# Kernel optimization log

Measured on AMD Instinct MI355X. Metric: run time of the kernel, lower is better.

Reference implementation:

```python
import jax, jax.numpy as jnp
from jax import lax
import numpy as np

GAMMA = 0.25        # inv_temp
C_SCALE = 1.0       # spectral_scale
STRIDE = 8          # patch stride (== patch_size, non-overlapping)


def setup_inputs() -> dict:
    key = jax.random.key(0)
    ks = jax.random.split(key, 9)
    B, C, H = 1024, 3, 64
    D, NP, M, NH, R, P = 256, 64, 1024, 8, 32, 8
    return {
        "x": jax.random.normal(ks[0], (B, C, H, H), jnp.float32),
        "z": jax.random.normal(ks[1], (B, NP, D), jnp.float32),
        "encoder_weight": jax.random.normal(ks[2], (D, C, P, P), jnp.float32) * 0.05,
        "encoder_bias": jax.random.normal(ks[3], (D,), jnp.float32) * 0.05,
        "visible_bias": jax.random.normal(ks[4], (C, H, H), jnp.float32) * 0.05,
        "pos_bias": jax.random.normal(ks[5], (NP, D), jnp.float32) * 0.05,
        "memory_weight": jax.random.normal(ks[6], (D, M), jnp.float32) * 0.05,
        "W_Q": jax.random.normal(ks[7], (NH, R, D), jnp.float32) * 0.05,
        "W_K": jax.random.normal(ks[8], (NH, R, D), jnp.float32) * 0.05,
    }


def reference(x, z, encoder_weight, encoder_bias, visible_bias, pos_bias,
              memory_weight, W_Q, W_K):
    """E = 0.5||x||^2 + 0.5||z||^2 - Phi_coupling(x, z); returns (B,)."""
    B = x.shape[0]
    D = encoder_weight.shape[0]

    quad_x = 0.5 * jnp.sum(x * x, axis=(1, 2, 3))
    quad_z = 0.5 * jnp.sum(z * z, axis=(1, 2))

    # visible-bias coupling
    phi_vis = jnp.sum(visible_bias[None] * x, axis=(1, 2, 3))

    # conv encode: (B, D, gh, gw) -> (B, NP, D)
    enc = lax.conv_general_dilated(
        x, C_SCALE * encoder_weight, window_strides=(STRIDE, STRIDE),
        padding='VALID', dimension_numbers=('NCHW', 'OIHW', 'NCHW'))
    encoded = enc.reshape(B, D, -1).transpose(0, 2, 1)  # (B, NP, D)

    # enc_act = 'none' -> identity
    phi_enc = jnp.sum(encoded * z, axis=(1, 2))
    phi_bias = jnp.sum(z * encoder_bias, axis=(1, 2))
    phi_pos = jnp.sum(z * pos_bias[None], axis=(1, 2))

    # memory ReLU^2 term: (B, NP, M)
    mem_proj = jnp.einsum('bpd,dm->bpm', z, C_SCALE * memory_weight)
    phi_mem = jnp.sum(jnp.square(jax.nn.relu(mem_proj)), axis=(1, 2))

    # Hopfield attention logsumexp term
    Q = jnp.einsum('bpd,hrd->bhrp', z, C_SCALE * W_Q)  # (B, H, R, NP)
    K = jnp.einsum('bpd,hrd->bhrp', z, C_SCALE * W_K)
    A = jnp.einsum('bhdm,bhdn->bhmn', Q, K)            # (B, H, NP, NP)
    phi_att = jnp.sum(jax.scipy.special.logsumexp(GAMMA * A, axis=-1),
                      axis=(1, 2)) / GAMMA

    coupling = phi_vis + phi_enc + phi_bias + phi_pos + phi_mem + phi_att
    return quad_x + quad_z - coupling
```

## Files before the change

### kernel.cpp

```cpp
#include <hip/hip_runtime.h>
#include <hip/hip_bf16.h>

#define GAMMA 0.25f


typedef __attribute__((ext_vector_type(8))) short short8;
typedef __attribute__((ext_vector_type(4))) float f32x4;

__device__ __forceinline__ float dot4(float4 a, float4 b) {
  return fmaf(a.x, b.x, fmaf(a.y, b.y, fmaf(a.z, b.z, a.w * b.w)));
}

__device__ __forceinline__ void fma4(float4& a, float s, float4 w) {
  a.x = fmaf(s, w.x, a.x); a.y = fmaf(s, w.y, a.y);
  a.z = fmaf(s, w.z, a.z); a.w = fmaf(s, w.w, a.w);
}

__device__ __forceinline__ ushort f2bf(float f) {
  __hip_bfloat16 h = __float2bfloat16(f);
  return *reinterpret_cast<ushort*>(&h);
}

__device__ __forceinline__ float bf2f(ushort u) {
  union { unsigned int i; float f; } v;
  v.i = ((unsigned int)u) << 16;
  return v.f;
}

__device__ __forceinline__ float block_sum_256(float v, float* tmp) {
#pragma unroll
  for (int off = 32; off; off >>= 1) v += __shfl_down(v, off, 64);
  int w = threadIdx.x >> 6;
  if ((threadIdx.x & 63) == 0) tmp[w] = v;
  __syncthreads();
  return tmp[0] + tmp[1] + tmp[2] + tmp[3];
}

__global__ __launch_bounds__(256) void k_cvt_weights_v5(
    const float* __restrict__ wq, const float* __restrict__ wk,
    const float* __restrict__ ew, const float* __restrict__ mw,
    ushort* __restrict__ wcf, ushort* __restrict__ ewt,
    ushort* __restrict__ mtf) {
  int bid = blockIdx.x, t = threadIdx.x;
  if (bid < 64) {
    int tid = bid * 256 + t;
    int frag = tid >> 6, l = tid & 63;
    int ctg = frag >> 3, kc = frag & 7;
    int col = ctg * 16 + (l & 15);
    int h = col >> 6, qk = (col >> 5) & 1, rr = col & 31;
    int k0 = kc * 32 + (l >> 4) * 8;
    const float* s = (qk ? wk : wq) + ((size_t)h * 32 + rr) * 256 + k0;
    float4 u = *(const float4*)s;
    float4 v = *(const float4*)(s + 4);
    ushort o[8];
    o[0] = f2bf(u.x); o[1] = f2bf(u.y); o[2] = f2bf(u.z); o[3] = f2bf(u.w);
    o[4] = f2bf(v.x); o[5] = f2bf(v.y); o[6] = f2bf(v.z); o[7] = f2bf(v.w);
    *(ushort4*)(wcf + (size_t)tid * 8) = *(ushort4*)&o[0];
    *(ushort4*)(wcf + (size_t)tid * 8 + 4) = *(ushort4*)&o[4];
  } else if (bid < 88) {
    int tid = (bid - 64) * 256 + t;
    int frag = tid >> 6, l = tid & 63;
    int ks = frag / 12, ct = frag % 12;
    const float* s = ew + (size_t)(ks * 32 + (l >> 4) * 8) * 192 +
                     ct * 16 + (l & 15);
    ushort o[8];
#pragma unroll
    for (int i = 0; i < 8; ++i) o[i] = f2bf(s[(size_t)i * 192]);
    *(ushort4*)(ewt + (size_t)tid * 8) = *(ushort4*)&o[0];
    *(ushort4*)(ewt + (size_t)tid * 8 + 4) = *(ushort4*)&o[4];
  } else {
    __shared__ ushort tile[32][264];
    int bid2 = bid - 88;
    int kc = bid2 >> 2, mg = bid2 & 3;
#pragma unroll
    for (int j = 0; j < 8; ++j) {
      int idx = t + j * 256;
      int kl = idx >> 6, m4 = idx & 63;
      float4 v = *(const float4*)(mw + (size_t)(kc * 32 + kl) * 1024 +
                                  mg * 256 + m4 * 4);
      ushort* dst = &tile[kl][m4 * 4];
      dst[0] = f2bf(v.x); dst[1] = f2bf(v.y);
      dst[2] = f2bf(v.z); dst[3] = f2bf(v.w);
    }
    __syncthreads();
#pragma unroll
    for (int j = 0; j < 4; ++j) {
      int e = t + j * 256;
      int fl = e >> 6, l2 = e & 63;
      int frag = (mg * 16 + fl) * 8 + kc;
      int m_loc = fl * 16 + (l2 & 15);
      ushort o[8];
#pragma unroll
      for (int i = 0; i < 8; ++i) o[i] = tile[(l2 >> 4) * 8 + i][m_loc];
      *(ushort4*)(mtf + ((size_t)frag * 64 + l2) * 8) = *(ushort4*)&o[0];
      *(ushort4*)(mtf + ((size_t)frag * 64 + l2) * 8 + 4) = *(ushort4*)&o[4];
    }
  }
}

__global__ __launch_bounds__(256) void k_mega(
    const float* __restrict__ z, const float* __restrict__ eb,
    const float* __restrict__ pb, const ushort* __restrict__ mtf,
    const ushort* __restrict__ wcf, float* __restrict__ out) {
  __shared__ ushort SL[32768];
  const int t = threadIdx.x, l = t & 63, w = t >> 6;
  const int b = blockIdx.x;
  const int q = l >> 4, m = l & 15;
  float s = 0.f;

  {
    const float4* zb4 = (const float4*)(z + (size_t)b * 16384);
    const float4* pb4 = (const float4*)pb;
    const float4* eb4 = (const float4*)eb;
#pragma unroll
    for (int n = 0; n < 16; ++n) {
      int i = t + n * 256;
      float4 zv = zb4[i];
      float4 pv = pb4[i];
      float4 ev = eb4[i & 63];
      float4 c;
      c.x = pv.x + ev.x; c.y = pv.y + ev.y;
      c.z = pv.z + ev.z; c.w = pv.w + ev.w;
      s += 0.5f * dot4(zv, zv) - dot4(zv, c);
      int p = i >> 6, d4 = i & 63;
      int ks = d4 >> 3, sub = (d4 & 7) >> 1, e0 = (d4 & 1) * 4;
      int li = (p & 15) + sub * 16;
      ushort4 o;
      o.x = f2bf(zv.x); o.y = f2bf(zv.y); o.z = f2bf(zv.z); o.w = f2bf(zv.w);
      *(ushort4*)(SL + (size_t)(((p >> 4) * 8 + ks) * 64 + li) * 8 + e0) = o;
    }
  }
  __syncthreads();

#pragma unroll 1
  for (int ct = 0; ct < 4; ++ct) {
    const ushort* Bb = mtf + ((size_t)(ct * 16 + w * 4) * 8) * 512 +
                       (size_t)l * 8;
    short8 fb[2][4];
#pragma unroll
    for (int c = 0; c < 4; ++c) fb[0][c] = *(const short8*)(Bb + (c * 8 + 0) * 512);
#pragma unroll
    for (int c = 0; c < 4; ++c) fb[1][c] = *(const short8*)(Bb + (c * 8 + 1) * 512);

    f32x4 acc[4][4];
#pragma unroll
    for (int r = 0; r < 4; ++r)
#pragma unroll
      for (int c = 0; c < 4; ++c) acc[r][c] = f32x4{0.f, 0.f, 0.f, 0.f};

#pragma unroll
    for (int kc = 0; kc < 8; ++kc) {
      const int cur = kc & 1;
      short8 a4[4];
#pragma unroll
      for (int r = 0; r < 4; ++r)
        a4[r] = *(const short8*)(SL + (size_t)((r * 8 + kc) * 64 + l) * 8);
#pragma unroll
      for (int r = 0; r < 4; ++r)
#pragma unroll
        for (int c = 0; c < 4; ++c)
          acc[r][c] = __builtin_amdgcn_mfma_f32_16x16x32_bf16(a4[r], fb[cur][c],
                                                              acc[r][c], 0, 0, 0);
      if (kc < 6) {
#pragma unroll
        for (int c = 0; c < 4; ++c)
          fb[cur][c] = *(const short8*)(Bb + (c * 8 + kc + 2) * 512);
      }
    }
#pragma unroll
    for (int r = 0; r < 4; ++r)
#pragma unroll
      for (int c = 0; c < 4; ++c)
#pragma unroll
        for (int e = 0; e < 4; ++e) {
          float rr = fmaxf(acc[r][c][e], 0.f);
          s -= rr * rr;
        }
  }

  float part = 0.f;
  char* dstg = (char*)(SL + 16384);
#pragma unroll 1
  for (int half = 0; half < 2; ++half) {
    const ushort* Bb = wcf + ((size_t)((half * 16 + w * 4) * 8)) * 512 +
                       (size_t)l * 8;
    short8 fb[2][4];
#pragma unroll
    for (int c = 0; c < 4; ++c) fb[0][c] = *(const short8*)(Bb + (c * 8 + 0) * 512);
#pragma unroll
    for (int c = 0; c < 4; ++c) fb[1][c] = *(const short8*)(Bb + (c * 8 + 1) * 512);

    f32x4 acc[4][4];
#pragma unroll
    for (int r = 0; r < 4; ++r)
#pragma unroll
      for (int c = 0; c < 4; ++c) acc[r][c] = f32x4{0.f, 0.f, 0.f, 0.f};

#pragma unroll
    for (int kc = 0; kc < 8; ++kc) {
      const int cur = kc & 1;
      short8 a4[4];
#pragma unroll
      for (int r = 0; r < 4; ++r)
        a4[r] = *(const short8*)(SL + (size_t)((r * 8 + kc) * 64 + l) * 8);
#pragma unroll
      for (int r = 0; r < 4; ++r)
#pragma unroll
        for (int c = 0; c < 4; ++c)
          acc[r][c] = __builtin_amdgcn_mfma_f32_16x16x32_bf16(a4[r], fb[cur][c],
                                                              acc[r][c], 0, 0, 0);
      if (kc < 6) {
#pragma unroll
        for (int c = 0; c < 4; ++c)
          fb[cur][c] = *(const short8*)(Bb + (c * 8 + kc + 2) * 512);
      }
    }

#pragma unroll
    for (int rt = 0; rt < 4; ++rt)
#pragma unroll
      for (int c = 0; c < 4; ++c)
#pragma unroll
        for (int reg = 0; reg < 4; ++reg) {
          int row = 16 * rt + 4 * q + reg;
          int col = (4 * w + c) * 16 + m;
          int ba = ((row * 256 + col) * 2) ^ ((row & 7) << 4);
          *(ushort*)(dstg + ba) = f2bf(acc[rt][c][reg]);
        }
    __syncthreads();

#pragma unroll
    for (int hh = 0; hh < 4; ++hh) {
      int rowq = 16 * w + m;
      short8 qa = *(const short8*)(
          dstg + (((rowq * 256 + hh * 64 + q * 8) * 2) ^ ((rowq & 7) << 4)));
      f32x4 a2[4];
#pragma unroll
      for (int nt = 0; nt < 4; ++nt) {
        int rowk = 16 * nt + m;
        short8 kb = *(const short8*)(
            dstg + (((rowk * 256 + hh * 64 + 32 + q * 8) * 2) ^ ((rowk & 7) << 4)));
        a2[nt] = __builtin_amdgcn_mfma_f32_16x16x32_bf16(
            qa, kb, f32x4{0.f, 0.f, 0.f, 0.f}, 0, 0, 0);
      }
#pragma unroll
      for (int reg = 0; reg < 4; ++reg) {
        float e = __expf(GAMMA * a2[0][reg]) + __expf(GAMMA * a2[1][reg]) +
                  __expf(GAMMA * a2[2][reg]) + __expf(GAMMA * a2[3][reg]);
        e += __shfl_xor(e, 1, 64);
        e += __shfl_xor(e, 2, 64);
        e += __shfl_xor(e, 4, 64);
        e += __shfl_xor(e, 8, 64);
        part += (m == 0) ? __logf(e) : 0.f;
      }
    }
    __syncthreads();
  }
  s -= part * (1.0f / GAMMA);

  float r = block_sum_256(s, (float*)SL);
  if (t == 0) out[b] = r;
}

__global__ __launch_bounds__(256) void k_enc_v5(
    const float* __restrict__ x, const float* __restrict__ vb,
    const float* __restrict__ z, const ushort* __restrict__ ewt,
    float* __restrict__ out) {
  __shared__ ushort xs[12288];
  __shared__ ushort ebuf[2][6144];
  __shared__ float tmp[4];
  const int b = blockIdx.x, t = threadIdx.x, l = t & 63, w = t >> 6;
  const int q = l >> 4, m = l & 15;

  const float* Zr = z + (size_t)b * 16384 + (size_t)(16 * w + m) * 256 + q * 8;
  short8 a[8];
#pragma unroll
  for (int ks = 0; ks < 8; ++ks) {
    float4 u = *(const float4*)(Zr + ks * 32);
    float4 v = *(const float4*)(Zr + ks * 32 + 4);
    ushort o[8];
    o[0] = f2bf(u.x); o[1] = f2bf(u.y); o[2] = f2bf(u.z); o[3] = f2bf(u.w);
    o[4] = f2bf(v.x); o[5] = f2bf(v.y); o[6] = f2bf(v.z); o[7] = f2bf(v.w);
    a[ks] = *(short8*)o;
  }

  short8 st[3];
#pragma unroll
  for (int i = 0; i < 3; ++i)
    st[i] = *(const short8*)(ewt + (size_t)(t + i * 256) * 8);

  const float4* xb = (const float4*)(x + (size_t)b * 12288);
  const float4* vb4 = (const float4*)vb;
  ushort4* xs4 = (ushort4*)xs;
  float s = 0.f;
  for (int i = t; i < 3072; i += 256) {
    float4 xv = xb[i];
    float4 bv = vb4[i];
    s += 0.5f * dot4(xv, xv) - dot4(bv, xv);
    ushort4 o;
    o.x = f2bf(xv.x); o.y = f2bf(xv.y); o.z = f2bf(xv.z); o.w = f2bf(xv.w);
    xs4[i] = o;
  }
#pragma unroll
  for (int i = 0; i < 3; ++i)
    *(short8*)(ebuf[0] + (size_t)(t + i * 256) * 8) = st[i];
  __syncthreads();

  f32x4 acc[12];
#pragma unroll
  for (int ct = 0; ct < 12; ++ct) acc[ct] = f32x4{0.f, 0.f, 0.f, 0.f};

#pragma unroll
  for (int ks = 0; ks < 8; ++ks) {
    const int cur = ks & 1;
    if (ks < 7) {
#pragma unroll
      for (int i = 0; i < 3; ++i)
        st[i] = *(const short8*)(ewt + (size_t)(ks + 1) * 6144 +
                                 (size_t)(t + i * 256) * 8);
    }
#pragma unroll
    for (int ct = 0; ct < 12; ++ct) {
      short8 bv = *(const short8*)(ebuf[cur] + (size_t)(ct * 64 + l) * 8);
      acc[ct] = __builtin_amdgcn_mfma_f32_16x16x32_bf16(a[ks], bv, acc[ct], 0, 0, 0);
    }
    if (ks < 7) {
#pragma unroll
      for (int i = 0; i < 3; ++i)
        *(short8*)(ebuf[cur ^ 1] + (size_t)(t + i * 256) * 8) = st[i];
    }
    __syncthreads();
  }

#pragma unroll
  for (int ct = 0; ct < 12; ++ct) {
#pragma unroll
    for (int reg = 0; reg < 4; ++reg) {
      const int p = 16 * w + 4 * q + reg, gi = p >> 3, gj = p & 7;
      const int k = ct * 16 + m, c = k >> 6, r2 = k & 63;
      const int ii = r2 >> 3, jj = r2 & 7;
      s -= acc[ct][reg] * bf2f(xs[c * 4096 + (gi * 8 + ii) * 64 + gj * 8 + jj]);
    }
  }
  float r = block_sum_256(s, tmp);
  if (t == 0) atomicAdd(out + b, r);
}

__global__ __launch_bounds__(256) void k_xz(const float* __restrict__ x,
                                            const float* __restrict__ z,
                                            const float* __restrict__ vb,
                                            const float* __restrict__ eb,
                                            const float* __restrict__ pb,
                                            float* __restrict__ out) {
  __shared__ float tmp[4];
  int b = blockIdx.x, t = threadIdx.x;
  const float4* xb = (const float4*)(x + (size_t)b * 12288);
  const float4* vb4 = (const float4*)vb;
  float s = 0.f;
  for (int i = t; i < 3072; i += 256) {
    float4 xv = xb[i];
    float4 bv = vb4[i];
    s += 0.5f * dot4(xv, xv) - dot4(bv, xv);
  }
  const float4* zb = (const float4*)(z + (size_t)b * 16384);
  const float4* pb4 = (const float4*)pb;
  const float4* eb4 = (const float4*)eb;
  for (int i = t; i < 4096; i += 256) {
    float4 zv = zb[i];
    float4 pv = pb4[i];
    float4 ev = eb4[i & 63];
    float4 c;
    c.x = pv.x + ev.x; c.y = pv.y + ev.y; c.z = pv.z + ev.z; c.w = pv.w + ev.w;
    s += 0.5f * dot4(zv, zv) - dot4(zv, c);
  }
  float r = block_sum_256(s, tmp);
  if (t == 0) out[b] = r;
}

__global__ __launch_bounds__(256) void k_enc(const float* __restrict__ x,
                                             const float* __restrict__ z,
                                             const float* __restrict__ ew,
                                             float* __restrict__ out) {
  __shared__ float xs[12288];
  __shared__ float tmp[4];
  int b = blockIdx.x, t = threadIdx.x;
  const float4* xb4 = (const float4*)(x + (size_t)b * 12288);
  for (int i = t; i < 3072; i += 256) ((float4*)xs)[i] = xb4[i];
  __syncthreads();

  float acc[64];
#pragma unroll
  for (int p = 0; p < 64; ++p) acc[p] = 0.f;

  for (int k4 = 0; k4 < 48; ++k4) {
    float4 wv = *(const float4*)(ew + (size_t)t * 192 + k4 * 4);
    int c = k4 >> 4;
    int ii = (k4 >> 1) & 7;
    int jh = (k4 & 1) * 4;
    const float* base = xs + c * 4096 + ii * 64 + jh;
#pragma unroll
    for (int p = 0; p < 64; ++p) {
      float4 pv = *(const float4*)(base + (p >> 3) * 512 + (p & 7) * 8);
      acc[p] = fmaf(wv.x, pv.x,
               fmaf(wv.y, pv.y, fmaf(wv.z, pv.z, fmaf(wv.w, pv.w, acc[p]))));
    }
  }
  const float* zb = z + (size_t)b * 16384;
  float s = 0.f;
#pragma unroll
  for (int p = 0; p < 64; ++p) s += acc[p] * zb[p * 256 + t];
  float r = block_sum_256(s, tmp);
  if (t == 0) atomicAdd(out + b, -r);
}

__global__ __launch_bounds__(256) void k_mem(const float* __restrict__ z,
                                             const float* __restrict__ mw,
                                             float* __restrict__ out) {
  __shared__ float zs[16 * 256];
  __shared__ float tmp[4];
  int b = blockIdx.x >> 2, pt = blockIdx.x & 3, t = threadIdx.x;
  const float4* zb4 = (const float4*)(z + (size_t)b * 16384 + pt * 4096);
  for (int i = t; i < 1024; i += 256) ((float4*)zs)[i] = zb4[i];
  __syncthreads();

  const float4* m4 = (const float4*)mw;
  float4 acc[16];
#pragma unroll
  for (int pp = 0; pp < 16; ++pp) acc[pp] = make_float4(0.f, 0.f, 0.f, 0.f);

#pragma unroll 2
  for (int k4 = 0; k4 < 64; ++k4) {
    float4 w0 = m4[(4 * k4 + 0) * 256 + t];
    float4 w1 = m4[(4 * k4 + 1) * 256 + t];
    float4 w2 = m4[(4 * k4 + 2) * 256 + t];
    float4 w3 = m4[(4 * k4 + 3) * 256 + t];
#pragma unroll
    for (int pp = 0; pp < 16; ++pp) {
      float4 zv = *(const float4*)&zs[pp * 256 + k4 * 4];
      fma4(acc[pp], zv.x, w0);
      fma4(acc[pp], zv.y, w1);
      fma4(acc[pp], zv.z, w2);
      fma4(acc[pp], zv.w, w3);
    }
  }
  float total = 0.f;
#pragma unroll
  for (int pp = 0; pp < 16; ++pp) {
    float r;
    r = fmaxf(acc[pp].x, 0.f); total = fmaf(r, r, total);
    r = fmaxf(acc[pp].y, 0.f); total = fmaf(r, r, total);
    r = fmaxf(acc[pp].z, 0.f); total = fmaf(r, r, total);
    r = fmaxf(acc[pp].w, 0.f); total = fmaf(r, r, total);
  }
  float r = block_sum_256(total, tmp);
  if (t == 0) atomicAdd(out + b, -r);
}

__global__ __launch_bounds__(256) void k_attn(const float* __restrict__ z,
                                              const float* __restrict__ wq,
                                              const float* __restrict__ wk,
                                              float* __restrict__ out) {
  __shared__ float lds[8192];
  __shared__ float red[4];
  const int b = blockIdx.x >> 1, half = blockIdx.x & 1;
  const int t = threadIdx.x;
  const int lane = t & 63;
  const int w = __builtin_amdgcn_readfirstlane(t >> 6);
  const float4* zb4 = (const float4*)(z + (size_t)b * 16384);

  float qa[4][8], ka[4][8];
#pragma unroll
  for (int hh = 0; hh < 4; ++hh)
#pragma unroll
    for (int j = 0; j < 8; ++j) { qa[hh][j] = 0.f; ka[hh][j] = 0.f; }

  float4* lds4 = (float4*)lds;
  for (int dc = 0; dc < 2; ++dc) {
    __syncthreads();
    for (int i = t; i < 2048; i += 256) {
      int p = i >> 5, ld4 = i & 31;
      lds4[ld4 * 64 + (p ^ (ld4 & 7))] = zb4[p * 64 + dc * 32 + ld4];
    }
    __syncthreads();
#pragma unroll
    for (int hh = 0; hh < 4; ++hh) {
      int h = half * 4 + hh;
      const float* Wqb = wq + (size_t)h * 8192 + (size_t)(w * 8) * 256 + dc * 128;
      const float* Wkb = wk + (size_t)h * 8192 + (size_t)(w * 8) * 256 + dc * 128;
      for (int ld4 = 0; ld4 < 32; ++ld4) {
        float4 wv[8], kv[8];
#pragma unroll
        for (int j = 0; j < 8; ++j) {
          wv[j] = *(const float4*)(Wqb + j * 256 + ld4 * 4);
          kv[j] = *(const float4*)(Wkb + j * 256 + ld4 * 4);
        }
        float4 zv = lds4[ld4 * 64 + (lane ^ (ld4 & 7))];
#pragma unroll
        for (int j = 0; j < 8; ++j) {
          qa[hh][j] = fmaf(wv[j].x, zv.x, fmaf(wv[j].y, zv.y,
                      fmaf(wv[j].z, zv.z, fmaf(wv[j].w, zv.w, qa[hh][j]))));
          ka[hh][j] = fmaf(kv[j].x, zv.x, fmaf(kv[j].y, zv.y,
                      fmaf(kv[j].z, zv.z, fmaf(kv[j].w, zv.w, ka[hh][j]))));
        }
      }
    }
  }

  float* Qs = lds;
  float* Ks = lds + 2048;
  float lse = 0.f;
#pragma unroll
  for (int hh = 0; hh < 4; ++hh) {
    __syncthreads();
#pragma unroll
    for (int j = 0; j < 8; ++j) {
      Qs[(w * 8 + j) * 64 + lane] = qa[hh][j];
      Ks[(w * 8 + j) * 64 + lane] = ka[hh][j];
    }
    __syncthreads();
    float av[16];
#pragma unroll
    for (int mm = 0; mm < 16; ++mm) av[mm] = 0.f;
    for (int rr = 0; rr < 32; ++rr) {
      float kv = Ks[rr * 64 + lane];
      const float* qrow = &Qs[rr * 64 + w * 16];
      float4 q0 = *(const float4*)(qrow + 0);
      float4 q1 = *(const float4*)(qrow + 4);
      float4 q2 = *(const float4*)(qrow + 8);
      float4 q3 = *(const float4*)(qrow + 12);
      av[0]  = fmaf(q0.x, kv, av[0]);  av[1]  = fmaf(q0.y, kv, av[1]);
      av[2]  = fmaf(q0.z, kv, av[2]);  av[3]  = fmaf(q0.w, kv, av[3]);
      av[4]  = fmaf(q1.x, kv, av[4]);  av[5]  = fmaf(q1.y, kv, av[5]);
      av[6]  = fmaf(q1.z, kv, av[6]);  av[7]  = fmaf(q1.w, kv, av[7]);
      av[8]  = fmaf(q2.x, kv, av[8]);  av[9]  = fmaf(q2.y, kv, av[9]);
      av[10] = fmaf(q2.z, kv, av[10]); av[11] = fmaf(q2.w, kv, av[11]);
      av[12] = fmaf(q3.x, kv, av[12]); av[13] = fmaf(q3.y, kv, av[13]);
      av[14] = fmaf(q3.z, kv, av[14]); av[15] = fmaf(q3.w, kv, av[15]);
    }
#pragma unroll
    for (int mm = 0; mm < 16; ++mm) {
      float e = __expf(GAMMA * av[mm]);
#pragma unroll
      for (int off = 32; off; off >>= 1) e += __shfl_xor(e, off, 64);
      lse += __logf(e);
    }
  }
  if (lane == 0) red[w] = lse;
  __syncthreads();
  if (t == 0)
    atomicAdd(out + b, -(red[0] + red[1] + red[2] + red[3]) * (1.0f / GAMMA));
}

extern "C" void kernel_launch(void* const* d_in, const int* in_sizes, int n_in,
                              void* d_out, int out_size, void* d_ws,
                              size_t ws_size, hipStream_t stream) {
  (void)in_sizes; (void)n_in; (void)out_size;
  const float* x  = (const float*)d_in[0];
  const float* z  = (const float*)d_in[1];
  const float* ew = (const float*)d_in[2];
  const float* eb = (const float*)d_in[3];
  const float* vb = (const float*)d_in[4];
  const float* pb = (const float*)d_in[5];
  const float* mw = (const float*)d_in[6];
  const float* wq = (const float*)d_in[7];
  const float* wk = (const float*)d_in[8];
  float* out = (float*)d_out;

  const size_t MT_B = (size_t)1024 * 256 * 2;
  const size_t WC_B = (size_t)512 * 256 * 2;
  const size_t EW_B = (size_t)96 * 64 * 8 * 2;
  const size_t FULL = MT_B + WC_B + EW_B;

  ushort* mtf = (ushort*)d_ws;
  ushort* wcf = (ushort*)((char*)d_ws + MT_B);
  ushort* ewt = (ushort*)((char*)d_ws + MT_B + WC_B);

  if (ws_size >= FULL) {
    k_cvt_weights_v5<<<120, 256, 0, stream>>>(wq, wk, ew, mw, wcf, ewt, mtf);
    k_mega  <<<1024, 256, 0, stream>>>(z, eb, pb, mtf, wcf, out);
    k_enc_v5<<<1024, 256, 0, stream>>>(x, vb, z, ewt, out);
  } else {
    k_xz  <<<1024, 256, 0, stream>>>(x, z, vb, eb, pb, out);
    k_enc <<<1024, 256, 0, stream>>>(x, z, ew, out);
    k_mem <<<4096, 256, 0, stream>>>(z, mw, out);
    k_attn<<<2048, 256, 0, stream>>>(z, wq, wk, out);
  }
}
```

Measured before the change: 221.6 us.

## Merge memory/attention and encoder kernels into one launch with interleaved block roles

Combines the mega (memory + attention) kernel and the encoder kernel into a single 2048-block launch. The block index picks the role and the batch, interleaving groups of 8 blocks so both kinds of work run at the same time on the GPU. Both roles now accumulate into the output with atomicAdd, which requires a memset of the output first. The aim is to drop a launch and its tail, and to overlap the MFMA-heavy blocks with the load-heavy ones. The cost is an extra memset and atomic traffic on every output, and both roles must share one LDS and register allocation.

```diff
diff --git a/kernel.cpp b/kernel.cpp
--- a/kernel.cpp
+++ b/kernel.cpp
@@ -98,250 +98,248 @@
   }
 }
 
-__global__ __launch_bounds__(256) void k_mega(
-    const float* __restrict__ z, const float* __restrict__ eb,
-    const float* __restrict__ pb, const ushort* __restrict__ mtf,
-    const ushort* __restrict__ wcf, float* __restrict__ out) {
+__global__ __launch_bounds__(256) void k_fused(
+    const float* __restrict__ x, const float* __restrict__ z,
+    const float* __restrict__ eb, const float* __restrict__ vb,
+    const float* __restrict__ pb, const ushort* __restrict__ ewt,
+    const ushort* __restrict__ mtf, const ushort* __restrict__ wcf,
+    float* __restrict__ out) {
   __shared__ ushort SL[32768];
+  __shared__ float tmp[4];
   const int t = threadIdx.x, l = t & 63, w = t >> 6;
-  const int b = blockIdx.x;
+  const int bid = blockIdx.x;
+  const int type = (bid >> 3) & 1;
+  const int b = ((bid >> 4) << 3) | (bid & 7);
   const int q = l >> 4, m = l & 15;
   float s = 0.f;
 
-  {
-    const float4* zb4 = (const float4*)(z + (size_t)b * 16384);
-    const float4* pb4 = (const float4*)pb;
-    const float4* eb4 = (const float4*)eb;
-#pragma unroll
-    for (int n = 0; n < 16; ++n) {
-      int i = t + n * 256;
-      float4 zv = zb4[i];
-      float4 pv = pb4[i];
-      float4 ev = eb4[i & 63];
-      float4 c;
-      c.x = pv.x + ev.x; c.y = pv.y + ev.y;
-      c.z = pv.z + ev.z; c.w = pv.w + ev.w;
-      s += 0.5f * dot4(zv, zv) - dot4(zv, c);
-      int p = i >> 6, d4 = i & 63;
-      int ks = d4 >> 3, sub = (d4 & 7) >> 1, e0 = (d4 & 1) * 4;
-      int li = (p & 15) + sub * 16;
+  if (type == 0) {
+    {
+      const float4* zb4 = (const float4*)(z + (size_t)b * 16384);
+      const float4* pb4 = (const float4*)pb;
+      const float4* eb4 = (const float4*)eb;
+#pragma unroll
+      for (int n = 0; n < 16; ++n) {
+        int i = t + n * 256;
+        float4 zv = zb4[i];
+        float4 pv = pb4[i];
+        float4 ev = eb4[i & 63];
+        float4 c;
+        c.x = pv.x + ev.x; c.y = pv.y + ev.y;
+        c.z = pv.z + ev.z; c.w = pv.w + ev.w;
+        s += 0.5f * dot4(zv, zv) - dot4(zv, c);
+        int p = i >> 6, d4 = i & 63;
+        int ks = d4 >> 3, sub = (d4 & 7) >> 1, e0 = (d4 & 1) * 4;
+        int li = (p & 15) + sub * 16;
+        ushort4 o;
+        o.x = f2bf(zv.x); o.y = f2bf(zv.y); o.z = f2bf(zv.z); o.w = f2bf(zv.w);
+        *(ushort4*)(SL + (size_t)(((p >> 4) * 8 + ks) * 64 + li) * 8 + e0) = o;
+      }
+    }
+    __syncthreads();
+
+#pragma unroll 1
+    for (int ct = 0; ct < 4; ++ct) {
+      const ushort* Bb = mtf + ((size_t)(ct * 16 + w * 4) * 8) * 512 +
+                         (size_t)l * 8;
+      short8 fb[2][4];
+#pragma unroll
+      for (int c = 0; c < 4; ++c) fb[0][c] = *(const short8*)(Bb + (c * 8 + 0) * 512);
+#pragma unroll
+      for (int c = 0; c < 4; ++c) fb[1][c] = *(const short8*)(Bb + (c * 8 + 1) * 512);
+
+      f32x4 acc[4][4];
+#pragma unroll
+      for (int r = 0; r < 4; ++r)
+#pragma unroll
+        for (int c = 0; c < 4; ++c) acc[r][c] = f32x4{0.f, 0.f, 0.f, 0.f};
+
+#pragma unroll
+      for (int kc = 0; kc < 8; ++kc) {
+        const int cur = kc & 1;
+        short8 a4[4];
+#pragma unroll
+        for (int r = 0; r < 4; ++r)
+          a4[r] = *(const short8*)(SL + (size_t)((r * 8 + kc) * 64 + l) * 8);
+#pragma unroll
+        for (int r = 0; r < 4; ++r)
+#pragma unroll
+          for (int c = 0; c < 4; ++c)
+            acc[r][c] = __builtin_amdgcn_mfma_f32_16x16x32_bf16(a4[r], fb[cur][c],
+                                                                acc[r][c], 0, 0, 0);
+        if (kc < 6) {
+#pragma unroll
+          for (int c = 0; c < 4; ++c)
+            fb[cur][c] = *(const short8*)(Bb + (c * 8 + kc + 2) * 512);
+        }
+      }
+#pragma unroll
+      for (int r = 0; r < 4; ++r)
+#pragma unroll
+        for (int c = 0; c < 4; ++c)
+#pragma unroll
+          for (int e = 0; e < 4; ++e) {
+            float rr = fmaxf(acc[r][c][e], 0.f);
+            s -= rr * rr;
+          }
+    }
+
+    float part = 0.f;
+    char* dstg = (char*)(SL + 16384);
+#pragma unroll 1
+    for (int half = 0; half < 2; ++half) {
+      const ushort* Bb = wcf + ((size_t)((half * 16 + w * 4) * 8)) * 512 +
+                         (size_t)l * 8;
+      short8 fb[2][4];
+#pragma unroll
+      for (int c = 0; c < 4; ++c) fb[0][c] = *(const short8*)(Bb + (c * 8 + 0) * 512);
+#pragma unroll
+      for (int c = 0; c < 4; ++c) fb[1][c] = *(const short8*)(Bb + (c * 8 + 1) * 512);
+
+      f32x4 acc[4][4];
+#pragma unroll
+      for (int r = 0; r < 4; ++r)
+#pragma unroll
+        for (int c = 0; c < 4; ++c) acc[r][c] = f32x4{0.f, 0.f, 0.f, 0.f};
+
+#pragma unroll
+      for (int kc = 0; kc < 8; ++kc) {
+        const int cur = kc & 1;
+        short8 a4[4];
+#pragma unroll
+        for (int r = 0; r < 4; ++r)
+          a4[r] = *(const short8*)(SL + (size_t)((r * 8 + kc) * 64 + l) * 8);
+#pragma unroll
+        for (int r = 0; r < 4; ++r)
+#pragma unroll
+          for (int c = 0; c < 4; ++c)
+            acc[r][c] = __builtin_amdgcn_mfma_f32_16x16x32_bf16(a4[r], fb[cur][c],
+                                                                acc[r][c], 0, 0, 0);
+        if (kc < 6) {
+#pragma unroll
+          for (int c = 0; c < 4; ++c)
+            fb[cur][c] = *(const short8*)(Bb + (c * 8 + kc + 2) * 512);
+        }
+      }
+
+#pragma unroll
+      for (int rt = 0; rt < 4; ++rt)
+#pragma unroll
+        for (int c = 0; c < 4; ++c)
+#pragma unroll
+          for (int reg = 0; reg < 4; ++reg) {
+            int row = 16 * rt + 4 * q + reg;
+            int col = (4 * w + c) * 16 + m;
+            int ba = ((row * 256 + col) * 2) ^ ((row & 7) << 4);
+            *(ushort*)(dstg + ba) = f2bf(acc[rt][c][reg]);
+          }
+      __syncthreads();
+
+#pragma unroll
+      for (int hh = 0; hh < 4; ++hh) {
+        int rowq = 16 * w + m;
+        short8 qa = *(const short8*)(
+            dstg + (((rowq * 256 + hh * 64 + q * 8) * 2) ^ ((rowq & 7) << 4)));
+        f32x4 a2[4];
+#pragma unroll
+        for (int nt = 0; nt < 4; ++nt) {
+          int rowk = 16 * nt + m;
+          short8 kb = *(const short8*)(
+              dstg + (((rowk * 256 + hh * 64 + 32 + q * 8) * 2) ^ ((rowk & 7) << 4)));
+          a2[nt] = __builtin_amdgcn_mfma_f32_16x16x32_bf16(
+              qa, kb, f32x4{0.f, 0.f, 0.f, 0.f}, 0, 0, 0);
+        }
+#pragma unroll
+        for (int reg = 0; reg < 4; ++reg) {
+          float e = __expf(GAMMA * a2[0][reg]) + __expf(GAMMA * a2[1][reg]) +
+                    __expf(GAMMA * a2[2][reg]) + __expf(GAMMA * a2[3][reg]);
+          e += __shfl_xor(e, 1, 64);
+          e += __shfl_xor(e, 2, 64);
+          e += __shfl_xor(e, 4, 64);
+          e += __shfl_xor(e, 8, 64);
+          part += (m == 0) ? __logf(e) : 0.f;
+        }
+      }
+      __syncthreads();
+    }
+    s -= part * (1.0f / GAMMA);
+  } else {
+    ushort* xs    = SL;
+    ushort* ebuf0 = SL + 12288;
+    ushort* ebuf1 = SL + 18432;
+
+    const float* Zr = z + (size_t)b * 16384 + (size_t)(16 * w + m) * 256 + q * 8;
+    short8 a[8];
+#pragma unroll
+    for (int ks = 0; ks < 8; ++ks) {
+      float4 u = *(const float4*)(Zr + ks * 32);
+      float4 v = *(const float4*)(Zr + ks * 32 + 4);
+      ushort o[8];
+      o[0] = f2bf(u.x); o[1] = f2bf(u.y); o[2] = f2bf(u.z); o[3] = f2bf(u.w);
+      o[4] = f2bf(v.x); o[5] = f2bf(v.y); o[6] = f2bf(v.z); o[7] = f2bf(v.w);
+      a[ks] = *(short8*)o;
+    }
+
+    short8 st[3];
+#pragma unroll
+    for (int i = 0; i < 3; ++i)
+      st[i] = *(const short8*)(ewt + (size_t)(t + i * 256) * 8);
+
+    const float4* xb = (const float4*)(x + (size_t)b * 12288);
+    const float4* vb4 = (const float4*)vb;
+    ushort4* xs4 = (ushort4*)xs;
+    for (int i = t; i < 3072; i += 256) {
+      float4 xv = xb[i];
+      float4 bv = vb4[i];
+      s += 0.5f * dot4(xv, xv) - dot4(bv, xv);
       ushort4 o;
-      o.x = f2bf(zv.x); o.y = f2bf(zv.y); o.z = f2bf(zv.z); o.w = f2bf(zv.w);
-      *(ushort4*)(SL + (size_t)(((p >> 4) * 8 + ks) * 64 + li) * 8 + e0) = o;
-    }
-  }
-  __syncthreads();
-
-#pragma unroll 1
-  for (int ct = 0; ct < 4; ++ct) {
-    const ushort* Bb = mtf + ((size_t)(ct * 16 + w * 4) * 8) * 512 +
-                       (size_t)l * 8;
-    short8 fb[2][4];
-#pragma unroll
-    for (int c = 0; c < 4; ++c) fb[0][c] = *(const short8*)(Bb + (c * 8 + 0) * 512);
-#pragma unroll
-    for (int c = 0; c < 4; ++c) fb[1][c] = *(const short8*)(Bb + (c * 8 + 1) * 512);
-
-    f32x4 acc[4][4];
-#pragma unroll
-    for (int r = 0; r < 4; ++r)
-#pragma unroll
-      for (int c = 0; c < 4; ++c) acc[r][c] = f32x4{0.f, 0.f, 0.f, 0.f};
-
-#pragma unroll
-    for (int kc = 0; kc < 8; ++kc) {
-      const int cur = kc & 1;
-      short8 a4[4];
-#pragma unroll
-      for (int r = 0; r < 4; ++r)
-        a4[r] = *(const short8*)(SL + (size_t)((r * 8 + kc) * 64 + l) * 8);
-#pragma unroll
-      for (int r = 0; r < 4; ++r)
-#pragma unroll
-        for (int c = 0; c < 4; ++c)
-          acc[r][c] = __builtin_amdgcn_mfma_f32_16x16x32_bf16(a4[r], fb[cur][c],
-                                                              acc[r][c], 0, 0, 0);
-      if (kc < 6) {
-#pragma unroll
-        for (int c = 0; c < 4; ++c)
-          fb[cur][c] = *(const short8*)(Bb + (c * 8 + kc + 2) * 512);
-      }
-    }
-#pragma unroll
-    for (int r = 0; r < 4; ++r)
-#pragma unroll
-      for (int c = 0; c < 4; ++c)
-#pragma unroll
-        for (int e = 0; e < 4; ++e) {
-          float rr = fmaxf(acc[r][c][e], 0.f);
-          s -= rr * rr;
-        }
-  }
-
-  float part = 0.f;
-  char* dstg = (char*)(SL + 16384);
-#pragma unroll 1
-  for (int half = 0; half < 2; ++half) {
-    const ushort* Bb = wcf + ((size_t)((half * 16 + w * 4) * 8)) * 512 +
-                       (size_t)l * 8;
-    short8 fb[2][4];
-#pragma unroll
-    for (int c = 0; c < 4; ++c) fb[0][c] = *(const short8*)(Bb + (c * 8 + 0) * 512);
-#pragma unroll
-    for (int c = 0; c < 4; ++c) fb[1][c] = *(const short8*)(Bb + (c * 8 + 1) * 512);
-
-    f32x4 acc[4][4];
-#pragma unroll
-    for (int r = 0; r < 4; ++r)
-#pragma unroll
-      for (int c = 0; c < 4; ++c) acc[r][c] = f32x4{0.f, 0.f, 0.f, 0.f};
-
-#pragma unroll
-    for (int kc = 0; kc < 8; ++kc) {
-      const int cur = kc & 1;
-      short8 a4[4];
-#pragma unroll
-      for (int r = 0; r < 4; ++r)
-        a4[r] = *(const short8*)(SL + (size_t)((r * 8 + kc) * 64 + l) * 8);
-#pragma unroll
-      for (int r = 0; r < 4; ++r)
-#pragma unroll
-        for (int c = 0; c < 4; ++c)
-          acc[r][c] = __builtin_amdgcn_mfma_f32_16x16x32_bf16(a4[r], fb[cur][c],
-                                                              acc[r][c], 0, 0, 0);
-      if (kc < 6) {
-#pragma unroll
-        for (int c = 0; c < 4; ++c)
-          fb[cur][c] = *(const short8*)(Bb + (c * 8 + kc + 2) * 512);
-      }
-    }
-
-#pragma unroll
-    for (int rt = 0; rt < 4; ++rt)
-#pragma unroll
-      for (int c = 0; c < 4; ++c)
-#pragma unroll
-        for (int reg = 0; reg < 4; ++reg) {
-          int row = 16 * rt + 4 * q + reg;
-          int col = (4 * w + c) * 16 + m;
-          int ba = ((row * 256 + col) * 2) ^ ((row & 7) << 4);
-          *(ushort*)(dstg + ba) = f2bf(acc[rt][c][reg]);
-        }
-    __syncthreads();
-
-#pragma unroll
-    for (int hh = 0; hh < 4; ++hh) {
-      int rowq = 16 * w + m;
-      short8 qa = *(const short8*)(
-          dstg + (((rowq * 256 + hh * 64 + q * 8) * 2) ^ ((rowq & 7) << 4)));
-      f32x4 a2[4];
-#pragma unroll
-      for (int nt = 0; nt < 4; ++nt) {
-        int rowk = 16 * nt + m;
-        short8 kb = *(const short8*)(
-            dstg + (((rowk * 256 + hh * 64 + 32 + q * 8) * 2) ^ ((rowk & 7) << 4)));
-        a2[nt] = __builtin_amdgcn_mfma_f32_16x16x32_bf16(
-            qa, kb, f32x4{0.f, 0.f, 0.f, 0.f}, 0, 0, 0);
-      }
+      o.x = f2bf(xv.x); o.y = f2bf(xv.y); o.z = f2bf(xv.z); o.w = f2bf(xv.w);
+      xs4[i] = o;
+    }
+#pragma unroll
+    for (int i = 0; i < 3; ++i)
+      *(short8*)(ebuf0 + (size_t)(t + i * 256) * 8) = st[i];
+    __syncthreads();
+
+    f32x4 acc[12];
+#pragma unroll
+    for (int ct = 0; ct < 12; ++ct) acc[ct] = f32x4{0.f, 0.f, 0.f, 0.f};
+
+#pragma unroll
+    for (int ks = 0; ks < 8; ++ks) {
+      ushort* eb_cur = (ks & 1) ? ebuf1 : ebuf0;
+      ushort* eb_nxt = (ks & 1) ? ebuf0 : ebuf1;
+      if (ks < 7) {
+#pragma unroll
+        for (int i = 0; i < 3; ++i)
+          st[i] = *(const short8*)(ewt + (size_t)(ks + 1) * 6144 +
+                                   (size_t)(t + i * 256) * 8);
+      }
+#pragma unroll
+      for (int ct = 0; ct < 12; ++ct) {
+        short8 bv = *(const short8*)(eb_cur + (size_t)(ct * 64 + l) * 8);
+        acc[ct] = __builtin_amdgcn_mfma_f32_16x16x32_bf16(a[ks], bv, acc[ct], 0, 0, 0);
+      }
+      if (ks < 7) {
+#pragma unroll
+        for (int i = 0; i < 3; ++i)
+          *(short8*)(eb_nxt + (size_t)(t + i * 256) * 8) = st[i];
+      }
+      __syncthreads();
+    }
+
+#pragma unroll
+    for (int ct = 0; ct < 12; ++ct) {
 #pragma unroll
       for (int reg = 0; reg < 4; ++reg) {
-        float e = __expf(GAMMA * a2[0][reg]) + __expf(GAMMA * a2[1][reg]) +
-                  __expf(GAMMA * a2[2][reg]) + __expf(GAMMA * a2[3][reg]);
-        e += __shfl_xor(e, 1, 64);
-        e += __shfl_xor(e, 2, 64);
-        e += __shfl_xor(e, 4, 64);
-        e += __shfl_xor(e, 8, 64);
-        part += (m == 0) ? __logf(e) : 0.f;
-      }
-    }
-    __syncthreads();
-  }
-  s -= part * (1.0f / GAMMA);
-
-  float r = block_sum_256(s, (float*)SL);
-  if (t == 0) out[b] = r;
-}
-
-__global__ __launch_bounds__(256) void k_enc_v5(
-    const float* __restrict__ x, const float* __restrict__ vb,
-    const float* __restrict__ z, const ushort* __restrict__ ewt,
-    float* __restrict__ out) {
-  __shared__ ushort xs[12288];
-  __shared__ ushort ebuf[2][6144];
-  __shared__ float tmp[4];
-  const int b = blockIdx.x, t = threadIdx.x, l = t & 63, w = t >> 6;
-  const int q = l >> 4, m = l & 15;
-
-  const float* Zr = z + (size_t)b * 16384 + (size_t)(16 * w + m) * 256 + q * 8;
-  short8 a[8];
-#pragma unroll
-  for (int ks = 0; ks < 8; ++ks) {
-    float4 u = *(const float4*)(Zr + ks * 32);
-    float4 v = *(const float4*)(Zr + ks * 32 + 4);
-    ushort o[8];
-    o[0] = f2bf(u.x); o[1] = f2bf(u.y); o[2] = f2bf(u.z); o[3] = f2bf(u.w);
-    o[4] = f2bf(v.x); o[5] = f2bf(v.y); o[6] = f2bf(v.z); o[7] = f2bf(v.w);
-    a[ks] = *(short8*)o;
-  }
-
-  short8 st[3];
-#pragma unroll
-  for (int i = 0; i < 3; ++i)
-    st[i] = *(const short8*)(ewt + (size_t)(t + i * 256) * 8);
-
-  const float4* xb = (const float4*)(x + (size_t)b * 12288);
-  const float4* vb4 = (const float4*)vb;
-  ushort4* xs4 = (ushort4*)xs;
-  float s = 0.f;
-  for (int i = t; i < 3072; i += 256) {
-    float4 xv = xb[i];
-    float4 bv = vb4[i];
-    s += 0.5f * dot4(xv, xv) - dot4(bv, xv);
-    ushort4 o;
-    o.x = f2bf(xv.x); o.y = f2bf(xv.y); o.z = f2bf(xv.z); o.w = f2bf(xv.w);
-    xs4[i] = o;
-  }
-#pragma unroll
-  for (int i = 0; i < 3; ++i)
-    *(short8*)(ebuf[0] + (size_t)(t + i * 256) * 8) = st[i];
-  __syncthreads();
-
-  f32x4 acc[12];
-#pragma unroll
-  for (int ct = 0; ct < 12; ++ct) acc[ct] = f32x4{0.f, 0.f, 0.f, 0.f};
-
-#pragma unroll
-  for (int ks = 0; ks < 8; ++ks) {
-    const int cur = ks & 1;
-    if (ks < 7) {
-#pragma unroll
-      for (int i = 0; i < 3; ++i)
-        st[i] = *(const short8*)(ewt + (size_t)(ks + 1) * 6144 +
-                                 (size_t)(t + i * 256) * 8);
-    }
-#pragma unroll
-    for (int ct = 0; ct < 12; ++ct) {
-      short8 bv = *(const short8*)(ebuf[cur] + (size_t)(ct * 64 + l) * 8);
-      acc[ct] = __builtin_amdgcn_mfma_f32_16x16x32_bf16(a[ks], bv, acc[ct], 0, 0, 0);
-    }
-    if (ks < 7) {
-#pragma unroll
-      for (int i = 0; i < 3; ++i)
-        *(short8*)(ebuf[cur ^ 1] + (size_t)(t + i * 256) * 8) = st[i];
-    }
-    __syncthreads();
-  }
-
-#pragma unroll
-  for (int ct = 0; ct < 12; ++ct) {
-#pragma unroll
-    for (int reg = 0; reg < 4; ++reg) {
-      const int p = 16 * w + 4 * q + reg, gi = p >> 3, gj = p & 7;
-      const int k = ct * 16 + m, c = k >> 6, r2 = k & 63;
-      const int ii = r2 >> 3, jj = r2 & 7;
-      s -= acc[ct][reg] * bf2f(xs[c * 4096 + (gi * 8 + ii) * 64 + gj * 8 + jj]);
-    }
-  }
+        const int p = 16 * w + 4 * q + reg, gi = p >> 3, gj = p & 7;
+        const int k = ct * 16 + m, c = k >> 6, r2 = k & 63;
+        const int ii = r2 >> 3, jj = r2 & 7;
+        s -= acc[ct][reg] * bf2f(xs[c * 4096 + (gi * 8 + ii) * 64 + gj * 8 + jj]);
+      }
+    }
+  }
+
   float r = block_sum_256(s, tmp);
   if (t == 0) atomicAdd(out + b, r);
 }
@@ -576,9 +574,9 @@
   ushort* ewt = (ushort*)((char*)d_ws + MT_B + WC_B);
 
   if (ws_size >= FULL) {
+    hipMemsetAsync(out, 0, 1024 * sizeof(float), stream);
     k_cvt_weights_v5<<<120, 256, 0, stream>>>(wq, wk, ew, mw, wcf, ewt, mtf);
-    k_mega  <<<1024, 256, 0, stream>>>(z, eb, pb, mtf, wcf, out);
-    k_enc_v5<<<1024, 256, 0, stream>>>(x, vb, z, ewt, out);
+    k_fused<<<2048, 256, 0, stream>>>(x, z, eb, vb, pb, ewt, mtf, wcf, out);
   } else {
     k_xz  <<<1024, 256, 0, stream>>>(x, z, vb, eb, pb, out);
     k_enc <<<1024, 256, 0, stream>>>(x, z, ew, out);
```

Result: slower. 235.3 us (+6.2%).
